# Kernel tuning notes

Hardware: AMD Instinct MI355X
Metric: run time of the kernel (lower is better)

Reference implementation:

```python
import jax, jax.numpy as jnp
import numpy as np

N = 50000        # nodes
E = 800000       # edges
H = 256          # hidden_dim == output_dim
L = 5            # num_layers
NUM_ATOM_F = 9   # OGB atom categorical features
NUM_BOND_F = 3   # OGB bond categorical features
ATOM_VOCAB = 64
BOND_VOCAB = 8
G = 128          # num graphs in batch
BN_EPS = 1e-5


def setup_inputs() -> dict:
    key = jax.random.key(0)
    ks = jax.random.split(key, 24)
    s = 0.02
    inp = {
        "x_feat": jax.random.randint(ks[0], (N, NUM_ATOM_F), 0, ATOM_VOCAB),
        "edge_index": jax.random.randint(ks[1], (2, E), 0, N),
        "edge_attr_raw": jax.random.randint(ks[2], (E, NUM_BOND_F), 0, BOND_VOCAB),
        "batch": jnp.sort(jax.random.randint(ks[3], (N,), 0, G)),
        "atom_emb": s * jax.random.normal(ks[4], (NUM_ATOM_F, ATOM_VOCAB, H), jnp.float32),
        "bond_emb": s * jax.random.normal(ks[5], (NUM_BOND_F, BOND_VOCAB, H), jnp.float32),
        # per-layer GINEConv MLP: Linear(H,H) -> BN -> relu -> Linear(H,H) -> relu
        "W1": s * jax.random.normal(ks[6], (L, H, H), jnp.float32),
        "b1": jnp.zeros((L, H), jnp.float32),
        "g1": jnp.ones((L, H), jnp.float32),
        "be1": jnp.zeros((L, H), jnp.float32),
        "W2": s * jax.random.normal(ks[7], (L, H, H), jnp.float32),
        "b2": jnp.zeros((L, H), jnp.float32),
        # outer per-layer BN
        "g2": jnp.ones((L, H), jnp.float32),
        "be2": jnp.zeros((L, H), jnp.float32),
        # output head: Linear -> BN -> relu -> Linear
        "outW1": s * jax.random.normal(ks[8], (H, H), jnp.float32),
        "outb1": jnp.zeros((H,), jnp.float32),
        "outg": jnp.ones((H,), jnp.float32),
        "outbe": jnp.zeros((H,), jnp.float32),
        "outW2": s * jax.random.normal(ks[9], (H, H), jnp.float32),
        "outb2": jnp.zeros((H,), jnp.float32),
    }
    return inp


def _bn(x, g, b):
    mu = jnp.mean(x, axis=0)
    var = jnp.var(x, axis=0)
    return (x - mu) * jax.lax.rsqrt(var + BN_EPS) * g + b


def reference(x_feat, edge_index, edge_attr_raw, batch,
              atom_emb, bond_emb, W1, b1, g1, be1, W2, b2, g2, be2,
              outW1, outb1, outg, outbe, outW2, outb2):
    # Atom/Bond encoders: sum of per-feature embeddings
    x = sum(atom_emb[f][x_feat[:, f]] for f in range(NUM_ATOM_F))        # [N,H]
    e = sum(bond_emb[f][edge_attr_raw[:, f]] for f in range(NUM_BOND_F))  # [E,H]
    src, dst = edge_index[0], edge_index[1]

    for i in range(L):
        # GINEConv: (1+eps)*x + sum_j relu(x_j + e_ij), eps=0
        m = jax.nn.relu(x[src] + e)                       # [E,H]
        agg = jax.ops.segment_sum(m, dst, num_segments=N)  # [N,H]
        h = x + agg
        h = jax.nn.relu(_bn(h @ W1[i] + b1[i], g1[i], be1[i]))
        h = jax.nn.relu(h @ W2[i] + b2[i])
        x = jax.nn.relu(_bn(h, g2[i], be2[i]))

    # output head + global_add_pool
    h = jax.nn.relu(_bn(x @ outW1 + outb1, outg, outbe))
    h = h @ outW2 + outb2
    return jax.ops.segment_sum(h, batch, num_segments=G)   # [G,H]
```

## Files before the change

### kernel.cpp

```cpp
#include <hip/hip_runtime.h>
#include <hip/hip_bf16.h>

#define NN 50000
#define EE 800000
#define HH 256
#define GG 128
#define LL 5
#define NCHUNK 196
#define BN_EPS 1e-5f

typedef __attribute__((ext_vector_type(8))) short short8_t;
typedef __attribute__((ext_vector_type(4))) float f32x4;
typedef __hip_bfloat16 bf16;

#define AS1 __attribute__((address_space(1)))
#define AS3 __attribute__((address_space(3)))

__device__ __forceinline__ float bf2f(unsigned short u) {
    unsigned int i = ((unsigned int)u) << 16;
    float f;
    __builtin_memcpy(&f, &i, 4);
    return f;
}
__device__ __forceinline__ unsigned short f2bf(float f) {
    bf16 h = __float2bfloat16(f);
    unsigned short u;
    __builtin_memcpy(&u, &h, 2);
    return u;
}

__global__ __launch_bounds__(256) void k_encode(const int* __restrict__ xf,
                                                const float* __restrict__ atom_emb,
                                                bf16* __restrict__ x) {
    int n = blockIdx.x, h = threadIdx.x;
    float s = 0.f;
#pragma unroll
    for (int f = 0; f < 9; ++f) {
        int v = xf[n * 9 + f];
        s += atom_emb[((size_t)f * 64 + v) * HH + h];
    }
    x[(size_t)n * HH + h] = __float2bfloat16(s);
}

__global__ __launch_bounds__(256) void k_combo(const float* __restrict__ bond_emb,
                                               bf16* __restrict__ table) {
    int c = blockIdx.x, h = threadIdx.x;
    float v = bond_emb[(size_t)((c >> 6) & 7) * HH + h]
            + bond_emb[(size_t)(8 + ((c >> 3) & 7)) * HH + h]
            + bond_emb[(size_t)(16 + (c & 7)) * HH + h];
    table[(size_t)c * HH + h] = __float2bfloat16(v);
}

__global__ __launch_bounds__(256) void k_prepw(const float* __restrict__ W1,
                                               const float* __restrict__ W2,
                                               const float* __restrict__ oW1,
                                               const float* __restrict__ oW2,
                                               bf16* __restrict__ out) {
    int z = blockIdx.z;
    const float* src = (z < 5) ? W1 + (size_t)z * 65536
                     : (z < 10) ? W2 + (size_t)(z - 5) * 65536
                     : (z == 10) ? oW1 : oW2;
    bf16* dst = out + (size_t)z * 65536;
    __shared__ float tile[32][33];
    int kt = blockIdx.y * 32, nt = blockIdx.x * 32;
    int tx = threadIdx.x, ty = threadIdx.y;
    for (int i = ty; i < 32; i += 8) tile[i][tx] = src[(size_t)(kt + i) * 256 + nt + tx];
    __syncthreads();
    for (int i = ty; i < 32; i += 8)
        dst[(size_t)(nt + i) * 256 + kt + tx] = __float2bfloat16(tile[tx][i]);
}

__global__ __launch_bounds__(256) void k_hist(const int* __restrict__ ei, int* __restrict__ deg) {
    int e = blockIdx.x * 256 + threadIdx.x;
    if (e < EE) atomicAdd(&deg[ei[EE + e]], 1);
}

__global__ __launch_bounds__(256) void k_scan_a(const int* __restrict__ deg, int* __restrict__ ro,
                                                int* __restrict__ bsum) {
    __shared__ int sm[256];
    int b = blockIdx.x, t = threadIdx.x;
    int idx = b * 256 + t;
    int v = (idx < NN) ? deg[idx] : 0;
    sm[t] = v;
    __syncthreads();
    for (int off = 1; off < 256; off <<= 1) {
        int add = (t >= off) ? sm[t - off] : 0;
        __syncthreads();
        sm[t] += add;
        __syncthreads();
    }
    if (idx <= NN) ro[idx] = sm[t] - v;
    if (t == 255) bsum[b] = sm[255];
}

__global__ __launch_bounds__(256) void k_scan_b(int* __restrict__ bsum) {
    __shared__ int sm[256];
    int t = threadIdx.x;
    int v = (t < NCHUNK) ? bsum[t] : 0;
    sm[t] = v;
    __syncthreads();
    for (int off = 1; off < 256; off <<= 1) {
        int add = (t >= off) ? sm[t - off] : 0;
        __syncthreads();
        sm[t] += add;
        __syncthreads();
    }
    if (t < NCHUNK) bsum[t] = sm[t] - v;
}

__global__ __launch_bounds__(256) void k_scan_c(int* __restrict__ ro, const int* __restrict__ bsum,
                                                int* __restrict__ cursor) {
    int b = blockIdx.x, t = threadIdx.x;
    int idx = b * 256 + t;
    if (idx <= NN) {
        int val = ro[idx] + bsum[b];
        ro[idx] = val;
        if (idx < NN) cursor[idx] = val;
    }
}

__global__ __launch_bounds__(256) void k_scatter(const int* __restrict__ ei,
                                                 const int* __restrict__ attr,
                                                 int* __restrict__ cursor,
                                                 int2* __restrict__ ebuf) {
    int e = blockIdx.x * 256 + threadIdx.x;
    if (e < EE) {
        int d = ei[EE + e];
        int c = (attr[e * 3] << 6) | (attr[e * 3 + 1] << 3) | attr[e * 3 + 2];
        int pos = atomicAdd(&cursor[d], 1);
        ebuf[pos] = make_int2(ei[e], c);
    }
}

__global__ __launch_bounds__(256) void k_bnrelu(bf16* __restrict__ t,
                                                const float* __restrict__ sIn,
                                                const float* __restrict__ qIn,
                                                const float* __restrict__ gIn,
                                                const float* __restrict__ beIn,
                                                float invN) {
    int grp = threadIdx.x >> 6;
    int lane = threadIdx.x & 63;
    int h4 = lane * 4;
    float4 s4 = *(const float4*)(sIn + h4);
    float4 q4 = *(const float4*)(qIn + h4);
    float4 g4 = *(const float4*)(gIn + h4);
    float4 b4 = *(const float4*)(beIn + h4);
    float4 cav, cbv;
#define COEF(C)                                                 \
    { float mu = s4.C * invN;                                   \
      float var = fmaf(-mu, mu, q4.C * invN);                   \
      float a = g4.C * rsqrtf(var + BN_EPS);                    \
      cav.C = a; cbv.C = fmaf(-mu, a, b4.C); }
    COEF(x) COEF(y) COEF(z) COEF(w)
#undef COEF
    for (int n = blockIdx.x * 4 + grp; n < NN; n += gridDim.x * 4) {
        ushort4 v = *(const ushort4*)(t + (size_t)n * HH + h4);
        ushort4 o;
        o.x = f2bf(fmaxf(fmaf(bf2f(v.x), cav.x, cbv.x), 0.f));
        o.y = f2bf(fmaxf(fmaf(bf2f(v.y), cav.y, cbv.y), 0.f));
        o.z = f2bf(fmaxf(fmaf(bf2f(v.z), cav.z, cbv.z), 0.f));
        o.w = f2bf(fmaxf(fmaf(bf2f(v.w), cav.w, cbv.w), 0.f));
        *(ushort4*)(t + (size_t)n * HH + h4) = o;
    }
}

__global__ __launch_bounds__(256) void k_aggregate(const bf16* __restrict__ u,
                                                   const int* __restrict__ ro,
                                                   const int2* __restrict__ eb,
                                                   const bf16* __restrict__ combo,
                                                   bf16* __restrict__ aggout) {
    int wid = threadIdx.x >> 6;
    int lane = threadIdx.x & 63;
    int half = lane >> 5;
    int sl = lane & 31;
    int n = blockIdx.x * 4 + wid;
    if (n >= NN) return;
    int h8 = sl * 8;
    float p0[8] = {0.f, 0.f, 0.f, 0.f, 0.f, 0.f, 0.f, 0.f};
    float p1[8] = {0.f, 0.f, 0.f, 0.f, 0.f, 0.f, 0.f, 0.f};
    int e0 = ro[n], e1 = ro[n + 1];
    int j = e0;
#define ACCUM(P, xs, cs)                                                       \
    {                                                                          \
        unsigned int xw[4] = {xs.x, xs.y, xs.z, xs.w};                         \
        unsigned int cw[4] = {cs.x, cs.y, cs.z, cs.w};                         \
        _Pragma("unroll") for (int q = 0; q < 4; ++q) {                        \
            float xlo = __uint_as_float(xw[q] << 16);                          \
            float xhi = __uint_as_float(xw[q] & 0xffff0000u);                  \
            float clo = __uint_as_float(cw[q] << 16);                          \
            float chi = __uint_as_float(cw[q] & 0xffff0000u);                  \
            P[2 * q] += fmaxf(xlo + clo, 0.f);                                 \
            P[2 * q + 1] += fmaxf(xhi + chi, 0.f);                             \
        }                                                                      \
    }
    for (; j + 4 <= e1; j += 4) {
        int2 rA = eb[j + half];
        int2 rB = eb[j + 2 + half];
        uint4 xA = *(const uint4*)(u + (size_t)rA.x * HH + h8);
        uint4 cA = *(const uint4*)(combo + ((size_t)rA.y << 8) + h8);
        uint4 xB = *(const uint4*)(u + (size_t)rB.x * HH + h8);
        uint4 cB = *(const uint4*)(combo + ((size_t)rB.y << 8) + h8);
        ACCUM(p0, xA, cA);
        ACCUM(p1, xB, cB);
    }
    for (; j < e1; j += 2) {
        int idx = j + half;
        bool v = idx < e1;
        int2 r = eb[v ? idx : e0];
        uint4 xA = *(const uint4*)(u + (size_t)r.x * HH + h8);
        uint4 cA = *(const uint4*)(combo + ((size_t)r.y << 8) + h8);
        if (v) ACCUM(p0, xA, cA);
    }
#undef ACCUM
#pragma unroll
    for (int i = 0; i < 8; ++i) {
        p0[i] += p1[i];
        p0[i] += __shfl_xor(p0[i], 32);
    }
    if (half == 0) {
        uint4 tv = *(const uint4*)(u + (size_t)n * HH + h8);
        unsigned int tw[4] = {tv.x, tv.y, tv.z, tv.w};
        unsigned int ow[4];
#pragma unroll
        for (int q = 0; q < 4; ++q) {
            float tlo = __uint_as_float(tw[q] << 16);
            float thi = __uint_as_float(tw[q] & 0xffff0000u);
            ow[q] = (unsigned int)f2bf(p0[2 * q] + tlo)
                  | ((unsigned int)f2bf(p0[2 * q + 1] + thi) << 16);
        }
        *(uint4*)(aggout + (size_t)n * HH + h8) = make_uint4(ow[0], ow[1], ow[2], ow[3]);
    }
}

struct GLds {
    uint4 a[2][512];
    uint4 b[2][1024];
    float ca[256], cb[256];
};

__device__ __forceinline__ uint4 xchunk(uint4 u, const float* ca, const float* cb, int k0) {
    float4 ca0 = *(const float4*)(ca + k0);
    float4 ca1 = *(const float4*)(ca + k0 + 4);
    float4 cb0 = *(const float4*)(cb + k0);
    float4 cb1 = *(const float4*)(cb + k0 + 4);
    float cav[8] = {ca0.x, ca0.y, ca0.z, ca0.w, ca1.x, ca1.y, ca1.z, ca1.w};
    float cbv[8] = {cb0.x, cb0.y, cb0.z, cb0.w, cb1.x, cb1.y, cb1.z, cb1.w};
    unsigned int s[4] = {u.x, u.y, u.z, u.w};
#pragma unroll
    for (int p = 0; p < 4; ++p) {
        float lo = bf2f((unsigned short)(s[p] & 0xffffu));
        float hi = bf2f((unsigned short)(s[p] >> 16));
        lo = fmaxf(fmaf(lo, cav[2 * p], cbv[2 * p]), 0.f);
        hi = fmaxf(fmaf(hi, cav[2 * p + 1], cbv[2 * p + 1]), 0.f);
        s[p] = (unsigned int)f2bf(lo) | ((unsigned int)f2bf(hi) << 16);
    }
    return make_uint4(s[0], s[1], s[2], s[3]);
}

template <bool HAS_T>
__global__ __launch_bounds__(512, 4) void k_gemm(const bf16* __restrict__ A,
                                                 const bf16* __restrict__ Wt,
                                                 const float* __restrict__ bias,
                                                 bf16* __restrict__ Out,
                                                 int M, int do_relu,
                                                 const float* __restrict__ sIn,
                                                 const float* __restrict__ qIn,
                                                 const float* __restrict__ gIn,
                                                 const float* __restrict__ beIn,
                                                 float invN,
                                                 float* __restrict__ ssum,
                                                 float* __restrict__ ssq) {
    __shared__ GLds L;
    const int t = threadIdx.x;
    const int lane = t & 63;
    const int w = t >> 6;
    const int wr = w >> 2, wc = w & 3;
    const int m0 = blockIdx.x * 128;
    const int lhi = lane >> 4, llo = lane & 15;

    if (HAS_T) {
        if (t < 256) {
            float mu = sIn[t] * invN;
            float var = fmaf(-mu, mu, qIn[t] * invN);
            float a = gIn[t] * rsqrtf(var + BN_EPS);
            L.ca[t] = a;
            L.cb[t] = fmaf(-mu, a, beIn[t]);
        }
        __syncthreads();
    }

    const int arow_i = t & 127, akg = t >> 7;
    const bf16* aptr = A + (size_t)(m0 + arow_i) * HH + akg * 8;
    const int bcol = wc * 64 + lane;
    const bf16* bptr = Wt + (size_t)bcol * HH + wr * 8;

    f32x4 acc[4][4] = {};
    uint4 areg, anext;

#define STAGE_B(c, kb)                                                                        \
    _Pragma("unroll") for (int q = 0; q < 2; ++q) {                                           \
        __builtin_amdgcn_global_load_lds((const AS1 void*)(bptr + (kb) + q * 16),             \
                                         (AS3 void*)&L.b[c][q * 512 + w * 64], 16, 0, 0);     \
    }
#define STAGE_A_DMA(c, kb)                                                                    \
    __builtin_amdgcn_global_load_lds((const AS1 void*)(aptr + (kb)),                          \
                                     (AS3 void*)&L.a[c][w * 64], 16, 0, 0);

    STAGE_B(0, 0);
    if (HAS_T) {
        areg = *(const uint4*)(aptr + 0);
        L.a[0][t] = xchunk(areg, L.ca, L.cb, akg * 8);
    } else {
        STAGE_A_DMA(0, 0);
    }
    __syncthreads();

    int c = 0;
    for (int step = 0; step < 8; ++step) {
        const int kn = (step + 1) * 32;
        if (step < 7) {
            STAGE_B(c ^ 1, kn);
            if (HAS_T) anext = *(const uint4*)(aptr + kn);
            else STAGE_A_DMA(c ^ 1, kn);
        }
        short8_t af[4], bfv[4];
#pragma unroll
        for (int m = 0; m < 4; ++m)
            af[m] = *(const short8_t*)&L.a[c][lhi * 128 + wr * 64 + m * 16 + llo];
#pragma unroll
        for (int n = 0; n < 4; ++n)
            bfv[n] = *(const short8_t*)&L.b[c][lhi * 256 + wc * 64 + n * 16 + llo];
#pragma unroll
        for (int m = 0; m < 4; ++m)
#pragma unroll
            for (int n = 0; n < 4; ++n)
                acc[m][n] = __builtin_amdgcn_mfma_f32_16x16x32_bf16(af[m], bfv[n], acc[m][n], 0, 0, 0);
        if (HAS_T && step < 7)
            L.a[c ^ 1][t] = xchunk(anext, L.ca, L.cb, kn + akg * 8);
        __syncthreads();
        c ^= 1;
    }
#undef STAGE_B
#undef STAGE_A_DMA

    float bias_n[4];
    int col_n[4];
#pragma unroll
    for (int n = 0; n < 4; ++n) {
        col_n[n] = wc * 64 + n * 16 + llo;
        bias_n[n] = bias[col_n[n]];
    }
    float ps[4] = {0.f, 0.f, 0.f, 0.f}, pq[4] = {0.f, 0.f, 0.f, 0.f};
#pragma unroll
    for (int m = 0; m < 4; ++m) {
#pragma unroll
        for (int j = 0; j < 4; ++j) {
            int row = m0 + wr * 64 + m * 16 + lhi * 4 + j;
            bool valid = row < M;
#pragma unroll
            for (int n = 0; n < 4; ++n) {
                float v = acc[m][n][j] + bias_n[n];
                if (do_relu) v = fmaxf(v, 0.f);
                if (valid) {
                    Out[(size_t)row * HH + col_n[n]] = __float2bfloat16(v);
                    ps[n] += v;
                    pq[n] = fmaf(v, v, pq[n]);
                }
            }
        }
    }

    if (ssum) {
#pragma unroll
        for (int n = 0; n < 4; ++n) {
            float s = ps[n];
            s += __shfl_xor(s, 16);
            s += __shfl_xor(s, 32);
            float q = pq[n];
            q += __shfl_xor(q, 16);
            q += __shfl_xor(q, 32);
            if (lhi == 0) {
                atomicAdd(&ssum[col_n[n]], s);
                atomicAdd(&ssq[col_n[n]], q);
            }
        }
    }
}

__global__ __launch_bounds__(256) void k_pool(const bf16* __restrict__ z,
                                              const int* __restrict__ batch,
                                              float* __restrict__ out) {
    int h = threadIdx.x;
    int n0 = blockIdx.x * 64;
    int n1 = n0 + 64;
    if (n1 > NN) n1 = NN;
    float s = 0.f;
    int g = batch[n0];
    for (int n = n0; n < n1; ++n) {
        int gn = batch[n];
        if (gn != g) {
            atomicAdd(&out[(size_t)g * HH + h], s);
            s = 0.f;
            g = gn;
        }
        s += bf2f(*(const unsigned short*)(z + (size_t)n * HH + h));
    }
    atomicAdd(&out[(size_t)g * HH + h], s);
}

static size_t align256(size_t v) { return (v + 255) & ~(size_t)255; }

extern "C" void kernel_launch(void* const* d_in, const int* in_sizes, int n_in,
                              void* d_out, int out_size, void* d_ws, size_t ws_size,
                              hipStream_t stream) {
    const int* x_feat = (const int*)d_in[0];
    const int* ei = (const int*)d_in[1];
    const int* attr = (const int*)d_in[2];
    const int* batch = (const int*)d_in[3];
    const float* atom_emb = (const float*)d_in[4];
    const float* bond_emb = (const float*)d_in[5];
    const float* W1 = (const float*)d_in[6];
    const float* b1 = (const float*)d_in[7];
    const float* g1 = (const float*)d_in[8];
    const float* be1 = (const float*)d_in[9];
    const float* W2 = (const float*)d_in[10];
    const float* b2 = (const float*)d_in[11];
    const float* g2 = (const float*)d_in[12];
    const float* be2 = (const float*)d_in[13];
    const float* outW1 = (const float*)d_in[14];
    const float* outb1 = (const float*)d_in[15];
    const float* outg = (const float*)d_in[16];
    const float* outbe = (const float*)d_in[17];
    const float* outW2 = (const float*)d_in[18];
    const float* outb2 = (const float*)d_in[19];
    float* out = (float*)d_out;

    char* ws = (char*)d_ws;
    const size_t BUF_STRIDE = align256((size_t)NN * HH * 2 + 131072);
    bf16* bufA = (bf16*)ws;
    bf16* bufB = (bf16*)(ws + BUF_STRIDE);
    bf16* bufC = (bf16*)(ws + 2 * BUF_STRIDE);
    char* p = ws + 3 * BUF_STRIDE;
    int2* ebuf = (int2*)p;            p += align256((size_t)EE * sizeof(int2));
    int* deg = (int*)p;               p += align256((size_t)NN * sizeof(int));
    int* ro = (int*)p;                p += align256((size_t)(NN + 1) * sizeof(int));
    int* cursor = (int*)p;            p += align256((size_t)NN * sizeof(int));
    int* bsum = (int*)p;              p += align256(256 * sizeof(int));
    float* stats = (float*)p;         p += align256(11 * 512 * sizeof(float));
    bf16* combo = (bf16*)p;           p += align256((size_t)512 * HH * sizeof(bf16));
    bf16* wbuf = (bf16*)p;            p += align256((size_t)12 * 65536 * sizeof(bf16));

    const float invN = 1.0f / (float)NN;
    const int EBLK = (EE + 255) / 256;
    const int GBLK = (NN + 127) / 128;
    const int AGG_GRID = (NN + 3) / 4;

    hipMemsetAsync(deg, 0, (size_t)NN * sizeof(int), stream);
    hipMemsetAsync(stats, 0, 11 * 512 * sizeof(float), stream);
    k_hist<<<EBLK, 256, 0, stream>>>(ei, deg);
    k_scan_a<<<NCHUNK, 256, 0, stream>>>(deg, ro, bsum);
    k_scan_b<<<1, 256, 0, stream>>>(bsum);
    k_scan_c<<<NCHUNK, 256, 0, stream>>>(ro, bsum, cursor);
    k_scatter<<<EBLK, 256, 0, stream>>>(ei, attr, cursor, ebuf);
    k_combo<<<512, 256, 0, stream>>>(bond_emb, combo);
    k_prepw<<<dim3(8, 8, 12), dim3(32, 8), 0, stream>>>(W1, W2, outW1, outW2, wbuf);
    k_encode<<<NN, 256, 0, stream>>>(x_feat, atom_emb, bufA);

    for (int l = 0; l < LL; ++l) {
        float* s1 = stats + (size_t)(2 * l) * 512;
        float* q1 = s1 + 256;
        float* s2 = stats + (size_t)(2 * l + 1) * 512;
        float* q2 = s2 + 256;
        if (l > 0) {
            float* sp = stats + (size_t)(2 * l - 1) * 512;
            k_bnrelu<<<2048, 256, 0, stream>>>(bufA, sp, sp + 256,
                                               g2 + (size_t)(l - 1) * HH,
                                               be2 + (size_t)(l - 1) * HH, invN);
        }
        k_aggregate<<<AGG_GRID, 256, 0, stream>>>(bufA, ro, ebuf, combo, bufB);
        k_gemm<false><<<GBLK, 512, 0, stream>>>(bufB, wbuf + (size_t)l * 65536,
                                                b1 + (size_t)l * HH, bufC, NN, 0,
                                                nullptr, nullptr, nullptr, nullptr,
                                                invN, s1, q1);
        k_gemm<true><<<GBLK, 512, 0, stream>>>(bufC, wbuf + (size_t)(5 + l) * 65536,
                                               b2 + (size_t)l * HH, bufA, NN, 1,
                                               s1, q1, g1 + (size_t)l * HH,
                                               be1 + (size_t)l * HH, invN, s2, q2);
    }

    float* sP = stats + (size_t)9 * 512;
    float* sH = stats + (size_t)10 * 512;
    float* qH = sH + 256;
    k_bnrelu<<<2048, 256, 0, stream>>>(bufA, sP, sP + 256,
                                       g2 + (size_t)4 * HH, be2 + (size_t)4 * HH, invN);
    k_gemm<false><<<GBLK, 512, 0, stream>>>(bufA, wbuf + (size_t)10 * 65536, outb1,
                                            bufB, NN, 0, nullptr, nullptr, nullptr, nullptr,
                                            invN, sH, qH);
    k_gemm<true><<<GBLK, 512, 0, stream>>>(bufB, wbuf + (size_t)11 * 65536, outb2,
                                           bufC, NN, 0, sH, qH, outg, outbe,
                                           invN, nullptr, nullptr);
    hipMemsetAsync(d_out, 0, (size_t)GG * HH * sizeof(float), stream);
    k_pool<<<(NN + 63) / 64, 256, 0, stream>>>(bufC, batch, out);
}
```

Baseline: 942.4 us.

## Fuse global add pool into final GEMM epilogue and merge memsets

The final output GEMM now accumulates its results directly into per-graph sums with atomics in its epilogue, using the sorted batch ids. This removes the separate pool kernel and the write and re-read of the final activation buffer. The two memsets are merged into one by placing the degree and stats buffers next to each other. The BN-relu kernel is changed from a grid-stride loop over a fixed grid to one node row per wave with a grid sized to the node count. The pooled epilogue issues more atomics from many blocks, and summing in fp32 instead of rounding to bf16 first changes numerics slightly.

```diff
diff --git a/kernel.cpp b/kernel.cpp
--- a/kernel.cpp
+++ b/kernel.cpp
@@ -153,15 +153,15 @@
       cav.C = a; cbv.C = fmaf(-mu, a, b4.C); }
     COEF(x) COEF(y) COEF(z) COEF(w)
 #undef COEF
-    for (int n = blockIdx.x * 4 + grp; n < NN; n += gridDim.x * 4) {
-        ushort4 v = *(const ushort4*)(t + (size_t)n * HH + h4);
-        ushort4 o;
-        o.x = f2bf(fmaxf(fmaf(bf2f(v.x), cav.x, cbv.x), 0.f));
-        o.y = f2bf(fmaxf(fmaf(bf2f(v.y), cav.y, cbv.y), 0.f));
-        o.z = f2bf(fmaxf(fmaf(bf2f(v.z), cav.z, cbv.z), 0.f));
-        o.w = f2bf(fmaxf(fmaf(bf2f(v.w), cav.w, cbv.w), 0.f));
-        *(ushort4*)(t + (size_t)n * HH + h4) = o;
-    }
+    int n = blockIdx.x * 4 + grp;
+    if (n >= NN) return;
+    ushort4 v = *(const ushort4*)(t + (size_t)n * HH + h4);
+    ushort4 o;
+    o.x = f2bf(fmaxf(fmaf(bf2f(v.x), cav.x, cbv.x), 0.f));
+    o.y = f2bf(fmaxf(fmaf(bf2f(v.y), cav.y, cbv.y), 0.f));
+    o.z = f2bf(fmaxf(fmaf(bf2f(v.z), cav.z, cbv.z), 0.f));
+    o.w = f2bf(fmaxf(fmaf(bf2f(v.w), cav.w, cbv.w), 0.f));
+    *(ushort4*)(t + (size_t)n * HH + h4) = o;
 }
 
 __global__ __launch_bounds__(256) void k_aggregate(const bf16* __restrict__ u,
@@ -257,7 +257,7 @@
     return make_uint4(s[0], s[1], s[2], s[3]);
 }
 
-template <bool HAS_T>
+template <bool HAS_T, bool POOL>
 __global__ __launch_bounds__(512, 4) void k_gemm(const bf16* __restrict__ A,
                                                  const bf16* __restrict__ Wt,
                                                  const float* __restrict__ bias,
@@ -269,7 +269,9 @@
                                                  const float* __restrict__ beIn,
                                                  float invN,
                                                  float* __restrict__ ssum,
-                                                 float* __restrict__ ssq) {
+                                                 float* __restrict__ ssq,
+                                                 const int* __restrict__ pbatch,
+                                                 float* __restrict__ pout) {
     __shared__ GLds L;
     const int t = threadIdx.x;
     const int lane = t & 63;
@@ -350,6 +352,41 @@
         col_n[n] = wc * 64 + n * 16 + llo;
         bias_n[n] = bias[col_n[n]];
     }
+
+    if (POOL) {
+        int gcur = -1;
+        float pacc[4] = {0.f, 0.f, 0.f, 0.f};
+#pragma unroll
+        for (int m = 0; m < 4; ++m) {
+#pragma unroll
+            for (int j = 0; j < 4; ++j) {
+                int row = m0 + wr * 64 + m * 16 + lhi * 4 + j;
+                if (row < M) {
+                    int g = pbatch[row];
+                    if (g != gcur) {
+                        if (gcur >= 0) {
+#pragma unroll
+                            for (int n = 0; n < 4; ++n)
+                                atomicAdd(&pout[(size_t)gcur * HH + col_n[n]], pacc[n]);
+                        }
+                        gcur = g;
+#pragma unroll
+                        for (int n = 0; n < 4; ++n) pacc[n] = 0.f;
+                    }
+#pragma unroll
+                    for (int n = 0; n < 4; ++n)
+                        pacc[n] += acc[m][n][j] + bias_n[n];
+                }
+            }
+        }
+        if (gcur >= 0) {
+#pragma unroll
+            for (int n = 0; n < 4; ++n)
+                atomicAdd(&pout[(size_t)gcur * HH + col_n[n]], pacc[n]);
+        }
+        return;
+    }
+
     float ps[4] = {0.f, 0.f, 0.f, 0.f}, pq[4] = {0.f, 0.f, 0.f, 0.f};
 #pragma unroll
     for (int m = 0; m < 4; ++m) {
@@ -385,27 +422,6 @@
             }
         }
     }
-}
-
-__global__ __launch_bounds__(256) void k_pool(const bf16* __restrict__ z,
-                                              const int* __restrict__ batch,
-                                              float* __restrict__ out) {
-    int h = threadIdx.x;
-    int n0 = blockIdx.x * 64;
-    int n1 = n0 + 64;
-    if (n1 > NN) n1 = NN;
-    float s = 0.f;
-    int g = batch[n0];
-    for (int n = n0; n < n1; ++n) {
-        int gn = batch[n];
-        if (gn != g) {
-            atomicAdd(&out[(size_t)g * HH + h], s);
-            s = 0.f;
-            g = gn;
-        }
-        s += bf2f(*(const unsigned short*)(z + (size_t)n * HH + h));
-    }
-    atomicAdd(&out[(size_t)g * HH + h], s);
 }
 
 static size_t align256(size_t v) { return (v + 255) & ~(size_t)255; }
@@ -442,11 +458,13 @@
     bf16* bufC = (bf16*)(ws + 2 * BUF_STRIDE);
     char* p = ws + 3 * BUF_STRIDE;
     int2* ebuf = (int2*)p;            p += align256((size_t)EE * sizeof(int2));
-    int* deg = (int*)p;               p += align256((size_t)NN * sizeof(int));
+    int* deg = (int*)p;
+    float* stats = (float*)(p + (size_t)NN * sizeof(int));
+    const size_t ZERO_BYTES = (size_t)NN * sizeof(int) + 11 * 512 * sizeof(float);
+    p += align256(ZERO_BYTES);
     int* ro = (int*)p;                p += align256((size_t)(NN + 1) * sizeof(int));
     int* cursor = (int*)p;            p += align256((size_t)NN * sizeof(int));
     int* bsum = (int*)p;              p += align256(256 * sizeof(int));
-    float* stats = (float*)p;         p += align256(11 * 512 * sizeof(float));
     bf16* combo = (bf16*)p;           p += align256((size_t)512 * HH * sizeof(bf16));
     bf16* wbuf = (bf16*)p;            p += align256((size_t)12 * 65536 * sizeof(bf16));
 
@@ -454,9 +472,9 @@
     const int EBLK = (EE + 255) / 256;
     const int GBLK = (NN + 127) / 128;
     const int AGG_GRID = (NN + 3) / 4;
-
-    hipMemsetAsync(deg, 0, (size_t)NN * sizeof(int), stream);
-    hipMemsetAsync(stats, 0, 11 * 512 * sizeof(float), stream);
+    const int BNR_GRID = (NN + 3) / 4;
+
+    hipMemsetAsync(deg, 0, ZERO_BYTES, stream);
     k_hist<<<EBLK, 256, 0, stream>>>(ei, deg);
     k_scan_a<<<NCHUNK, 256, 0, stream>>>(deg, ro, bsum);
     k_scan_b<<<1, 256, 0, stream>>>(bsum);
@@ -473,32 +491,32 @@
         float* q2 = s2 + 256;
         if (l > 0) {
             float* sp = stats + (size_t)(2 * l - 1) * 512;
-            k_bnrelu<<<2048, 256, 0, stream>>>(bufA, sp, sp + 256,
-                                               g2 + (size_t)(l - 1) * HH,
-                                               be2 + (size_t)(l - 1) * HH, invN);
+            k_bnrelu<<<BNR_GRID, 256, 0, stream>>>(bufA, sp, sp + 256,
+                                                   g2 + (size_t)(l - 1) * HH,
+                                                   be2 + (size_t)(l - 1) * HH, invN);
         }
         k_aggregate<<<AGG_GRID, 256, 0, stream>>>(bufA, ro, ebuf, combo, bufB);
-        k_gemm<false><<<GBLK, 512, 0, stream>>>(bufB, wbuf + (size_t)l * 65536,
-                                                b1 + (size_t)l * HH, bufC, NN, 0,
-                                                nullptr, nullptr, nullptr, nullptr,
-                                                invN, s1, q1);
-        k_gemm<true><<<GBLK, 512, 0, stream>>>(bufC, wbuf + (size_t)(5 + l) * 65536,
-                                               b2 + (size_t)l * HH, bufA, NN, 1,
-                                               s1, q1, g1 + (size_t)l * HH,
-                                               be1 + (size_t)l * HH, invN, s2, q2);
+        k_gemm<false, false><<<GBLK, 512, 0, stream>>>(bufB, wbuf + (size_t)l * 65536,
+                                                       b1 + (size_t)l * HH, bufC, NN, 0,
+                                                       nullptr, nullptr, nullptr, nullptr,
+                                                       invN, s1, q1, nullptr, nullptr);
+        k_gemm<true, false><<<GBLK, 512, 0, stream>>>(bufC, wbuf + (size_t)(5 + l) * 65536,
+                                                      b2 + (size_t)l * HH, bufA, NN, 1,
+                                                      s1, q1, g1 + (size_t)l * HH,
+                                                      be1 + (size_t)l * HH, invN, s2, q2,
+                                                      nullptr, nullptr);
     }
 
     float* sP = stats + (size_t)9 * 512;
     float* sH = stats + (size_t)10 * 512;
     float* qH = sH + 256;
-    k_bnrelu<<<2048, 256, 0, stream>>>(bufA, sP, sP + 256,
-                                       g2 + (size_t)4 * HH, be2 + (size_t)4 * HH, invN);
-    k_gemm<false><<<GBLK, 512, 0, stream>>>(bufA, wbuf + (size_t)10 * 65536, outb1,
-                                            bufB, NN, 0, nullptr, nullptr, nullptr, nullptr,
-                                            invN, sH, qH);
-    k_gemm<true><<<GBLK, 512, 0, stream>>>(bufB, wbuf + (size_t)11 * 65536, outb2,
-                                           bufC, NN, 0, sH, qH, outg, outbe,
-                                           invN, nullptr, nullptr);
+    k_bnrelu<<<BNR_GRID, 256, 0, stream>>>(bufA, sP, sP + 256,
+                                           g2 + (size_t)4 * HH, be2 + (size_t)4 * HH, invN);
+    k_gemm<false, false><<<GBLK, 512, 0, stream>>>(bufA, wbuf + (size_t)10 * 65536, outb1,
+                                                   bufB, NN, 0, nullptr, nullptr, nullptr,
+                                                   nullptr, invN, sH, qH, nullptr, nullptr);
     hipMemsetAsync(d_out, 0, (size_t)GG * HH * sizeof(float), stream);
-    k_pool<<<(NN + 63) / 64, 256, 0, stream>>>(bufC, batch, out);
-}
+    k_gemm<true, true><<<GBLK, 512, 0, stream>>>(bufB, wbuf + (size_t)11 * 65536, outb2,
+                                                 bufC, NN, 0, sH, qH, outg, outbe,
+                                                 invN, nullptr, nullptr, batch, out);
+}
```

After: 941.2 us. Within noise of the previous version (-0.1%).
